# Kernel tuning notes

Measured on AMD Instinct MI355X. Metric: run time of the kernel, lower is better.

Reference implementation:

```python
import jax, jax.numpy as jnp
import numpy as np

N = 100_000   # nodes
E = 1_600_000 # edges
IN, H, OUT = 128, 128, 128
G = 64        # graphs in batch
EPS = 1e-5    # batchnorm eps


def setup_inputs() -> dict:
    key = jax.random.key(0)
    ks = jax.random.split(key, 16)
    x = jax.random.normal(ks[0], (N, IN), dtype=jnp.float32)
    edge_index = jax.random.randint(ks[1], (2, E), 0, N, dtype=jnp.int32)
    batch = jnp.sort(jax.random.randint(ks[2], (N,), 0, G, dtype=jnp.int32))
    def lin(k, fi, fo):
        return jax.random.normal(k, (fi, fo), dtype=jnp.float32) / np.sqrt(fi).astype(np.float32)
    inp = {
        'x': x, 'edge_index': edge_index, 'batch': batch,
        'W1': lin(ks[3], IN, H), 'b1': jnp.zeros((H,), jnp.float32),
        'g1': jnp.ones((H,), jnp.float32), 'beta1': jnp.zeros((H,), jnp.float32),
        'W2': lin(ks[4], H, H), 'b2': jnp.zeros((H,), jnp.float32),
        'g2': jnp.ones((H,), jnp.float32), 'beta2': jnp.zeros((H,), jnp.float32),
        'W3': lin(ks[5], H, H), 'b3': jnp.zeros((H,), jnp.float32),
        'g3': jnp.ones((H,), jnp.float32), 'beta3': jnp.zeros((H,), jnp.float32),
        'fc_w': lin(ks[6], H, OUT), 'fc_b': jnp.zeros((OUT,), jnp.float32),
    }
    return inp


def _gcn_prep(edge_index):
    # add self loops, compute symmetric normalization (shared across layers)
    loop = jnp.arange(N, dtype=edge_index.dtype)
    row = jnp.concatenate([edge_index[0], loop])  # source
    col = jnp.concatenate([edge_index[1], loop])  # target
    deg = jax.ops.segment_sum(jnp.ones_like(col, dtype=jnp.float32), col, num_segments=N)
    dinv = jnp.where(deg > 0, jax.lax.rsqrt(deg), 0.0)
    norm = dinv[row] * dinv[col]  # (E+N,)
    return row, col, norm


def _gcn_bn_relu(h, W, b, g, beta, row, col, norm):
    hw = h @ W                                           # (N, H)
    msg = norm[:, None] * hw[row]                        # gather + scale
    h = jax.ops.segment_sum(msg, col, num_segments=N) + b  # scatter-add
    # BatchNorm1d (training-mode batch statistics, biased var)
    mu = jnp.mean(h, axis=0)
    var = jnp.mean(jnp.square(h - mu), axis=0)
    h = g * (h - mu) * jax.lax.rsqrt(var + EPS) + beta
    return jax.nn.relu(h)


def reference(x, edge_index, batch, W1, b1, g1, beta1, W2, b2, g2, beta2,
              W3, b3, g3, beta3, fc_w, fc_b):
    row, col, norm = _gcn_prep(edge_index)
    h = _gcn_bn_relu(x, W1, b1, g1, beta1, row, col, norm)
    h = _gcn_bn_relu(h, W2, b2, g2, beta2, row, col, norm)
    h = _gcn_bn_relu(h, W3, b3, g3, beta3, row, col, norm)
    # global_mean_pool over batch assignment
    sums = jax.ops.segment_sum(h, batch, num_segments=G)
    cnt = jax.ops.segment_sum(jnp.ones((N,), jnp.float32), batch, num_segments=G)
    pooled = sums / jnp.maximum(cnt, 1.0)[:, None]       # (G, H)
    return pooled @ fc_w + fc_b                          # (G, OUT)
```

## Files before the change

kernel.cpp:

```cpp
#include <hip/hip_runtime.h>

#define NN 100000
#define EE 1600000
#define HH 128
#define GG 64
#define TOT (EE + NN)
#define PSPLIT 8
#define NB 782
#define BCAP 4096
#define FCHUNK 4096

typedef __attribute__((ext_vector_type(8))) short s16x8;
typedef __attribute__((ext_vector_type(4))) float f32x4;

__device__ __forceinline__ unsigned short f2bf(float f) {
    unsigned u = __float_as_uint(f);
    u = u + 0x7FFFu + ((u >> 16) & 1u);
    return (unsigned short)(u >> 16);
}


__global__ __launch_bounds__(256) void setup_kernel(const float* __restrict__ x,
                                                    const int* __restrict__ batch,
                                                    const float* __restrict__ W0,
                                                    const float* __restrict__ W1,
                                                    const float* __restrict__ W2,
                                                    unsigned* __restrict__ Xbf,
                                                    int* __restrict__ cursor,
                                                    int* __restrict__ gstart, int* __restrict__ gend,
                                                    float* __restrict__ poolsum,
                                                    unsigned short* __restrict__ Wt) {
    int i = blockIdx.x * 256 + threadIdx.x;
    if (i < NN * 64) {
        float2 v = ((const float2*)x)[i];
        Xbf[i] = (unsigned)f2bf(v.x) | ((unsigned)f2bf(v.y) << 16);
    }
    if (i < NB) cursor[i] = i * BCAP;
    if (i < GG * HH) poolsum[i] = 0.f;
    if (i < GG) {
        int lo = 0, hi = NN;
        while (lo < hi) { int m = (lo + hi) >> 1; if (batch[m] < i) lo = m + 1; else hi = m; }
        int s = lo;
        lo = 0; hi = NN;
        while (lo < hi) { int m = (lo + hi) >> 1; if (batch[m] < i + 1) lo = m + 1; else hi = m; }
        gstart[i] = s;
        gend[i] = lo;
    }
    if (i < 3 * HH * HH) {
        int l = i >> 14, r = i & 16383;
        const float* W = (l == 0) ? W0 : (l == 1) ? W1 : W2;
        int k = r >> 7, n = r & 127;
        int dst = ((((n >> 4) * 16 + (k >> 5) * 4 + ((k >> 3) & 3)) * 16) + (n & 15)) * 8 + (k & 7);
        Wt[l * HH * HH + dst] = f2bf(W[r]);
    }
}

__global__ __launch_bounds__(256) void bfill2_kernel(const int* __restrict__ ei, int* cursor,
                                                     unsigned* __restrict__ ebuf) {
    __shared__ int h[NB];
    __shared__ int lbase[NB];
    int tid = threadIdx.x;
    size_t e0 = (size_t)blockIdx.x * FCHUNK;
    for (int i = tid; i < NB; i += 256) h[i] = 0;
    __syncthreads();
    unsigned r[16], c[16];
#pragma unroll
    for (int k = 0; k < 16; ++k) {
        size_t e = e0 + (size_t)k * 256 + tid;
        unsigned rr = 0xFFFFFFFFu, cc = 0;
        if (e < EE) {
            rr = (unsigned)ei[e];
            cc = (unsigned)ei[EE + e];
            if (rr >= NN || cc >= NN) rr = 0xFFFFFFFFu;
        }
        r[k] = rr; c[k] = cc;
        if (rr != 0xFFFFFFFFu) atomicAdd(&h[cc >> 7], 1);
    }
    __syncthreads();
    for (int i = tid; i < NB; i += 256) {
        int cnt = h[i];
        lbase[i] = cnt ? atomicAdd(&cursor[i], cnt) : 0;
    }
    __syncthreads();
    for (int i = tid; i < NB; i += 256) h[i] = 0;
    __syncthreads();
#pragma unroll
    for (int k = 0; k < 16; ++k) {
        if (r[k] != 0xFFFFFFFFu) {
            unsigned cc = c[k];
            int b = cc >> 7;
            int slot = lbase[b] + atomicAdd(&h[b], 1);
            if (slot >= b * BCAP && slot < (b + 1) * BCAP)
                ebuf[slot] = (r[k] << 7) | (cc & 127u);
        }
    }
}

__global__ void bscan_kernel(const int* __restrict__ cursor, int* __restrict__ bucketSlotStart,
                             int* __restrict__ col_start) {
    __shared__ int ss[1024];
    int t = threadIdx.x;
    int ec = 0, nc = 0;
    if (t < NB) {
        ec = min(max(cursor[t] - t * BCAP, 0), BCAP);
        nc = min(128, NN - t * 128);
    }
    ss[t] = ec + nc;
    __syncthreads();
    for (int off = 1; off < 1024; off <<= 1) {
        int a = 0;
        if (t >= off) a = ss[t - off];
        __syncthreads();
        ss[t] += a;
        __syncthreads();
    }
    if (t < NB) bucketSlotStart[t] = ss[t] - (ec + nc);
    if (t == NB - 1) col_start[NN] = ss[t];
}

__global__ __launch_bounds__(256) void bproc_kernel(const unsigned* __restrict__ ebuf,
                                                    const int* __restrict__ cursor,
                                                    const int* __restrict__ bucketSlotStart,
                                                    int* __restrict__ col_start,
                                                    float* __restrict__ dinv,
                                                    int* __restrict__ srcv) {
    __shared__ unsigned s_e[BCAP];
    __shared__ int s_cnt[128], s_scan[128], s_cur[128];
    int b = blockIdx.x;
    int tid = threadIdx.x;
    int n0 = b * 128;
    int nb = min(128, NN - n0);
    int est = b * BCAP;
    int ecnt = min(max(cursor[b] - est, 0), BCAP);
    if (tid < 128) s_cnt[tid] = 0;
    __syncthreads();
    for (int i = tid; i < ecnt; i += 256) {
        unsigned v = ebuf[est + i];
        s_e[i] = v;
        atomicAdd(&s_cnt[v & 127u], 1);
    }
    __syncthreads();
    int myc = 0;
    if (tid < 128) {
        myc = (tid < nb) ? s_cnt[tid] + 1 : 0;
        s_scan[tid] = myc;
    }
    __syncthreads();
    for (int off = 1; off < 128; off <<= 1) {
        int a = 0;
        if (tid < 128 && tid >= off) a = s_scan[tid - off];
        __syncthreads();
        if (tid < 128) s_scan[tid] += a;
        __syncthreads();
    }
    if (tid < nb) {
        int slotbase = bucketSlotStart[b] + s_scan[tid] - myc;
        col_start[n0 + tid] = slotbase;
        dinv[n0 + tid] = rsqrtf((float)(s_cnt[tid] + 1));
        srcv[slotbase] = n0 + tid;
        s_cur[tid] = slotbase + 1;
    }
    __syncthreads();
    for (int i = tid; i < ecnt; i += 256) {
        unsigned v = s_e[i];
        int slot = atomicAdd(&s_cur[v & 127u], 1);
        srcv[slot] = (int)(v >> 7);
    }
}


__global__ __launch_bounds__(256) void agg_kernel(const uint4* __restrict__ Xbf4,
                                                  const int* __restrict__ col_start,
                                                  const int* __restrict__ srcv,
                                                  const float* __restrict__ dinv,
                                                  unsigned short* __restrict__ Abf,
                                                  float* __restrict__ gsum,
                                                  float* __restrict__ gsq) {
    if (blockIdx.x == 0 && threadIdx.x < HH) {
        gsum[threadIdx.x] = 0.f;
        gsq[threadIdx.x] = 0.f;
    }
    int wv = (int)((blockIdx.x * blockDim.x + threadIdx.x) >> 6);
    int lane = threadIdx.x & 63;
    int half = lane >> 5;
    int node = 2 * wv + half;
    if (2 * wv >= NN) return;
    bool valid = node < NN;
    int s0 = 0, s1 = 0;
    float dd = 0.f;
    if (valid) { s0 = col_start[node]; s1 = col_start[node + 1]; dd = dinv[node]; }
    int lane31 = lane & 31;
    int qh = (lane >> 4) & 1;
    int l16 = lane & 15;
    float acc[8];
#pragma unroll
    for (int j = 0; j < 8; ++j) acc[j] = 0.f;

    for (int base = s0; base < s1; base += 32) {
        int cnt = min(32, s1 - base);
        int msrc = 0;
        float mw = 0.f;
        if (lane31 < cnt) { msrc = srcv[base + lane31]; mw = dinv[msrc] * dd; }
        int rounds = (cnt + 1) >> 1;
        int rp = ((rounds + 5) / 6) * 6;
        for (int p = 0; p < rp; p += 6) {
            uint4 u[6];
            float w[6];
#pragma unroll
            for (int k = 0; k < 6; ++k) {
                int idx = (p + k) * 2 + qh;
                int sl = half * 32 + min(idx, 31);
                int src = __shfl(msrc, sl);
                float wk = __shfl(mw, sl);
                if (idx > 31) wk = 0.f;
                w[k] = wk;
                u[k] = Xbf4[(size_t)src * 16 + l16];
            }
#pragma unroll
            for (int k = 0; k < 6; ++k) {
                acc[0] += w[k] * __uint_as_float(u[k].x << 16);
                acc[1] += w[k] * __uint_as_float(u[k].x & 0xFFFF0000u);
                acc[2] += w[k] * __uint_as_float(u[k].y << 16);
                acc[3] += w[k] * __uint_as_float(u[k].y & 0xFFFF0000u);
                acc[4] += w[k] * __uint_as_float(u[k].z << 16);
                acc[5] += w[k] * __uint_as_float(u[k].z & 0xFFFF0000u);
                acc[6] += w[k] * __uint_as_float(u[k].w << 16);
                acc[7] += w[k] * __uint_as_float(u[k].w & 0xFFFF0000u);
            }
        }
    }
#pragma unroll
    for (int j = 0; j < 8; ++j) acc[j] += __shfl_xor(acc[j], 16);
    if ((lane & 16) == 0 && valid) {
        uint4 pk;
        pk.x = (unsigned)f2bf(acc[0]) | ((unsigned)f2bf(acc[1]) << 16);
        pk.y = (unsigned)f2bf(acc[2]) | ((unsigned)f2bf(acc[3]) << 16);
        pk.z = (unsigned)f2bf(acc[4]) | ((unsigned)f2bf(acc[5]) << 16);
        pk.w = (unsigned)f2bf(acc[6]) | ((unsigned)f2bf(acc[7]) << 16);
        ((uint4*)Abf)[(size_t)node * 16 + l16] = pk;
    }
}

__global__ __launch_bounds__(256) void gemm_stats_kernel(const unsigned short* __restrict__ Abf,
                                                         const unsigned short* __restrict__ Wf,
                                                         const float* __restrict__ bias,
                                                         float* __restrict__ gsum,
                                                         float* __restrict__ gsq) {
    __shared__ float ssum[HH], ssq[HH];
    int tid = threadIdx.x;
    if (tid < HH) { ssum[tid] = 0.f; ssq[tid] = 0.f; }
    __syncthreads();

    int lane = tid & 63;
    int wave = tid >> 6;
    int mcol = lane & 15;
    int quad = lane >> 4;
    int rowbase = blockIdx.x * 128 + wave * 32;
    int row0 = rowbase + mcol;
    int row1 = row0 + 16;

    f32x4 acc[2][8];
#pragma unroll
    for (int mt = 0; mt < 2; ++mt)
#pragma unroll
        for (int nt = 0; nt < 8; ++nt) acc[mt][nt] = (f32x4){0.f, 0.f, 0.f, 0.f};

    s16x8 zf = {0, 0, 0, 0, 0, 0, 0, 0};
#pragma unroll
    for (int ks = 0; ks < 4; ++ks) {
        int k0 = ks * 32 + quad * 8;
        s16x8 a0 = (row0 < NN) ? *(const s16x8*)(Abf + (size_t)row0 * HH + k0) : zf;
        s16x8 a1 = (row1 < NN) ? *(const s16x8*)(Abf + (size_t)row1 * HH + k0) : zf;
#pragma unroll
        for (int nt = 0; nt < 8; ++nt) {
            s16x8 b = *(const s16x8*)(Wf + (((nt * 16 + ks * 4 + quad) * 16 + mcol) << 3));
            acc[0][nt] = __builtin_amdgcn_mfma_f32_16x16x32_bf16(a0, b, acc[0][nt], 0, 0, 0);
            acc[1][nt] = __builtin_amdgcn_mfma_f32_16x16x32_bf16(a1, b, acc[1][nt], 0, 0, 0);
        }
    }

    float s[8], sq[8];
#pragma unroll
    for (int nt = 0; nt < 8; ++nt) { s[nt] = 0.f; sq[nt] = 0.f; }
#pragma unroll
    for (int mt = 0; mt < 2; ++mt) {
        int rbase = rowbase + mt * 16 + quad * 4;
#pragma unroll
        for (int nt = 0; nt < 8; ++nt) {
            float bv = bias[nt * 16 + mcol];
            f32x4 a = acc[mt][nt];
#pragma unroll
            for (int reg = 0; reg < 4; ++reg) {
                if (rbase + reg < NN) {
                    float h = a[reg] + bv;
                    s[nt] += h; sq[nt] += h * h;
                }
            }
        }
    }
#pragma unroll
    for (int nt = 0; nt < 8; ++nt) {
        float v = s[nt];  v += __shfl_xor(v, 16);  v += __shfl_xor(v, 32);
        float w = sq[nt]; w += __shfl_xor(w, 16);  w += __shfl_xor(w, 32);
        if (quad == 0) {
            atomicAdd(&ssum[nt * 16 + mcol], v);
            atomicAdd(&ssq[nt * 16 + mcol], w);
        }
    }
    __syncthreads();
    if (tid < HH) {
        atomicAdd(&gsum[tid], ssum[tid]);
        atomicAdd(&gsq[tid], ssq[tid]);
    }
}

__global__ __launch_bounds__(256) void gemm_apply_kernel(const unsigned short* __restrict__ Abf,
                                                         const unsigned short* __restrict__ Wf,
                                                         const float* __restrict__ bias,
                                                         const float* __restrict__ gsum,
                                                         const float* __restrict__ gsq,
                                                         const float* __restrict__ g,
                                                         const float* __restrict__ beta,
                                                         unsigned short* __restrict__ Xb16) {
    __shared__ float asc[HH], bsh[HH];
    int tid = threadIdx.x;
    if (tid < HH) {
        float mu = gsum[tid] * (1.f / (float)NN);
        float var = fmaxf(gsq[tid] * (1.f / (float)NN) - mu * mu, 0.f);
        float a = g[tid] * rsqrtf(var + 1e-5f);
        asc[tid] = a;
        bsh[tid] = a * (bias[tid] - mu) + beta[tid];
    }
    __syncthreads();

    int lane = tid & 63;
    int wave = tid >> 6;
    int mcol = lane & 15;
    int quad = lane >> 4;
    int rowbase = blockIdx.x * 128 + wave * 32;
    int row0 = rowbase + mcol;
    int row1 = row0 + 16;

    f32x4 acc[2][8];
#pragma unroll
    for (int mt = 0; mt < 2; ++mt)
#pragma unroll
        for (int nt = 0; nt < 8; ++nt) acc[mt][nt] = (f32x4){0.f, 0.f, 0.f, 0.f};

    s16x8 zf = {0, 0, 0, 0, 0, 0, 0, 0};
#pragma unroll
    for (int ks = 0; ks < 4; ++ks) {
        int k0 = ks * 32 + quad * 8;
        s16x8 a0 = (row0 < NN) ? *(const s16x8*)(Abf + (size_t)row0 * HH + k0) : zf;
        s16x8 a1 = (row1 < NN) ? *(const s16x8*)(Abf + (size_t)row1 * HH + k0) : zf;
#pragma unroll
        for (int nt = 0; nt < 8; ++nt) {
            s16x8 b = *(const s16x8*)(Wf + (((nt * 16 + ks * 4 + quad) * 16 + mcol) << 3));
            acc[0][nt] = __builtin_amdgcn_mfma_f32_16x16x32_bf16(a0, b, acc[0][nt], 0, 0, 0);
            acc[1][nt] = __builtin_amdgcn_mfma_f32_16x16x32_bf16(a1, b, acc[1][nt], 0, 0, 0);
        }
    }

#pragma unroll
    for (int mt = 0; mt < 2; ++mt) {
        int rbase = rowbase + mt * 16 + quad * 4;
#pragma unroll
        for (int nt = 0; nt < 8; ++nt) {
            int col = nt * 16 + mcol;
            float av = asc[col], bv = bsh[col];
            f32x4 a = acc[mt][nt];
#pragma unroll
            for (int reg = 0; reg < 4; ++reg) {
                int r = rbase + reg;
                if (r < NN) {
                    float o = fmaxf(av * a[reg] + bv, 0.f);
                    Xb16[(size_t)r * HH + col] = f2bf(o);
                }
            }
        }
    }
}


__global__ void pool_kernel(const unsigned* __restrict__ Xbf, const int* __restrict__ gstart,
                            const int* __restrict__ gend, float* __restrict__ poolsum) {
    int g = blockIdx.x;
    int sp = blockIdx.y;
    int t = threadIdx.x;
    int s = gstart[g], e = gend[g];
    if (e <= s) return;
    int len = e - s;
    int chunk = (len + PSPLIT - 1) / PSPLIT;
    int cs = s + sp * chunk;
    int ce = min(cs + chunk, e);
    if (cs >= ce) return;
    float2 acc = make_float2(0.f, 0.f);
    for (int i = cs; i < ce; ++i) {
        unsigned u = Xbf[(size_t)i * 64 + t];
        acc.x += __uint_as_float(u << 16);
        acc.y += __uint_as_float(u & 0xFFFF0000u);
    }
    atomicAdd(&poolsum[g * HH + 2 * t], acc.x);
    atomicAdd(&poolsum[g * HH + 2 * t + 1], acc.y);
}

__global__ void fc_kernel(const float* __restrict__ poolsum, const int* __restrict__ gstart,
                          const int* __restrict__ gend, const float* __restrict__ fc_w,
                          const float* __restrict__ fc_b, float* __restrict__ out) {
    int g = blockIdx.x;
    int o = threadIdx.x;
    int cnt = gend[g] - gstart[g];
    float inv = (cnt > 0) ? (1.f / (float)cnt) : 0.f;
    float acc = fc_b[o];
    for (int k = 0; k < HH; ++k) acc += (poolsum[g * HH + k] * inv) * fc_w[k * HH + o];
    out[g * HH + o] = acc;
}


extern "C" void kernel_launch(void* const* d_in, const int* in_sizes, int n_in,
                              void* d_out, int out_size, void* d_ws, size_t ws_size,
                              hipStream_t stream) {
    const float* x     = (const float*)d_in[0];
    const int*   ei    = (const int*)d_in[1];
    const int*   batch = (const int*)d_in[2];
    const float* Wl[3]    = {(const float*)d_in[3], (const float*)d_in[7], (const float*)d_in[11]};
    const float* bl[3]    = {(const float*)d_in[4], (const float*)d_in[8], (const float*)d_in[12]};
    const float* gl[3]    = {(const float*)d_in[5], (const float*)d_in[9], (const float*)d_in[13]};
    const float* betal[3] = {(const float*)d_in[6], (const float*)d_in[10], (const float*)d_in[14]};
    const float* fc_w = (const float*)d_in[15];
    const float* fc_b = (const float*)d_in[16];
    float* out = (float*)d_out;

    char* ws = (char*)d_ws;
    size_t off = 0;
    auto take = [&](size_t n) -> void* {
        void* p = ws + off;
        off = (off + n + 255) & ~(size_t)255;
        return p;
    };
    int*   bucketSlotStart = (int*)take((size_t)NB * 4);
    int*   cursor          = (int*)take((size_t)NB * 4);
    unsigned* ebuf         = (unsigned*)take((size_t)NB * BCAP * 4);
    int*   col_start       = (int*)take((size_t)(NN + 1) * 4);
    float* dinv            = (float*)take((size_t)NN * 4);
    int*   srcv            = (int*)take((size_t)TOT * 4);
    float* gsum            = (float*)take(HH * 4);
    float* gsq             = (float*)take(HH * 4);
    int*   gstart          = (int*)take(GG * 4);
    int*   gend            = (int*)take(GG * 4);
    float* poolsum         = (float*)take((size_t)GG * HH * 4);
    unsigned short* wt     = (unsigned short*)take((size_t)3 * HH * HH * 2);
    unsigned* Xbf          = (unsigned*)take((size_t)NN * 64 * 4);
    unsigned short* Abf    = (unsigned short*)take((size_t)NN * HH * 2);

    setup_kernel<<<(NN * 64 + 255) / 256, 256, 0, stream>>>(x, batch, Wl[0], Wl[1], Wl[2],
                                                            Xbf, cursor, gstart, gend, poolsum, wt);
    bfill2_kernel<<<(EE + FCHUNK - 1) / FCHUNK, 256, 0, stream>>>(ei, cursor, ebuf);
    bscan_kernel<<<1, 1024, 0, stream>>>(cursor, bucketSlotStart, col_start);
    bproc_kernel<<<NB, 256, 0, stream>>>(ebuf, cursor, bucketSlotStart, col_start, dinv, srcv);

    const int aggBlocks = (((NN + 1) / 2) * 64 + 255) / 256;
    for (int l = 0; l < 3; ++l) {
        const unsigned short* W = wt + (size_t)l * HH * HH;
        agg_kernel<<<aggBlocks, 256, 0, stream>>>((const uint4*)Xbf, col_start, srcv,
                                                  dinv, Abf, gsum, gsq);
        gemm_stats_kernel<<<(NN + 127) / 128, 256, 0, stream>>>(Abf, W, bl[l], gsum, gsq);
        gemm_apply_kernel<<<(NN + 127) / 128, 256, 0, stream>>>(Abf, W, bl[l], gsum, gsq,
                                                                gl[l], betal[l],
                                                                (unsigned short*)Xbf);
    }

    pool_kernel<<<dim3(GG, PSPLIT), 64, 0, stream>>>(Xbf, gstart, gend, poolsum);
    fc_kernel<<<GG, 128, 0, stream>>>(poolsum, gstart, gend, fc_w, fc_b, out);
}
```

Baseline: 550.3 us.

## Build CSR via global degree atomics and direct atomic scatter

Replaces the bucketed edge-buffer CSR construction with a global atomic degree count fused into setup, a block-level scan, a per-node prefix pass, and an atomic scatter of sources into CSR slots. It removes the intermediate ebuf round trip and its fixed-capacity buckets. In exchange it uses global atomics on 100K counters, which may contend, and edge order within rows becomes nondeterministic. The single-block scan now serially sums degrees per thread.

```diff
diff --git a/kernel.cpp b/kernel.cpp
--- a/kernel.cpp
+++ b/kernel.cpp
@@ -7,8 +7,6 @@
 #define TOT (EE + NN)
 #define PSPLIT 8
 #define NB 782
-#define BCAP 4096
-#define FCHUNK 4096
 
 typedef __attribute__((ext_vector_type(8))) short s16x8;
 typedef __attribute__((ext_vector_type(4))) float f32x4;
@@ -21,12 +19,13 @@
 
 
 __global__ __launch_bounds__(256) void setup_kernel(const float* __restrict__ x,
+                                                    const int* __restrict__ ei,
                                                     const int* __restrict__ batch,
                                                     const float* __restrict__ W0,
                                                     const float* __restrict__ W1,
                                                     const float* __restrict__ W2,
                                                     unsigned* __restrict__ Xbf,
-                                                    int* __restrict__ cursor,
+                                                    int* __restrict__ deg,
                                                     int* __restrict__ gstart, int* __restrict__ gend,
                                                     float* __restrict__ poolsum,
                                                     unsigned short* __restrict__ Wt) {
@@ -35,7 +34,10 @@
         float2 v = ((const float2*)x)[i];
         Xbf[i] = (unsigned)f2bf(v.x) | ((unsigned)f2bf(v.y) << 16);
     }
-    if (i < NB) cursor[i] = i * BCAP;
+    if (i < EE) {
+        unsigned r = (unsigned)ei[i], c = (unsigned)ei[EE + i];
+        if (r < NN && c < NN) atomicAdd(&deg[c], 1);
+    }
     if (i < GG * HH) poolsum[i] = 0.f;
     if (i < GG) {
         int lo = 0, hi = NN;
@@ -55,57 +57,17 @@
     }
 }
 
-__global__ __launch_bounds__(256) void bfill2_kernel(const int* __restrict__ ei, int* cursor,
-                                                     unsigned* __restrict__ ebuf) {
-    __shared__ int h[NB];
-    __shared__ int lbase[NB];
-    int tid = threadIdx.x;
-    size_t e0 = (size_t)blockIdx.x * FCHUNK;
-    for (int i = tid; i < NB; i += 256) h[i] = 0;
-    __syncthreads();
-    unsigned r[16], c[16];
-#pragma unroll
-    for (int k = 0; k < 16; ++k) {
-        size_t e = e0 + (size_t)k * 256 + tid;
-        unsigned rr = 0xFFFFFFFFu, cc = 0;
-        if (e < EE) {
-            rr = (unsigned)ei[e];
-            cc = (unsigned)ei[EE + e];
-            if (rr >= NN || cc >= NN) rr = 0xFFFFFFFFu;
-        }
-        r[k] = rr; c[k] = cc;
-        if (rr != 0xFFFFFFFFu) atomicAdd(&h[cc >> 7], 1);
-    }
-    __syncthreads();
-    for (int i = tid; i < NB; i += 256) {
-        int cnt = h[i];
-        lbase[i] = cnt ? atomicAdd(&cursor[i], cnt) : 0;
-    }
-    __syncthreads();
-    for (int i = tid; i < NB; i += 256) h[i] = 0;
-    __syncthreads();
-#pragma unroll
-    for (int k = 0; k < 16; ++k) {
-        if (r[k] != 0xFFFFFFFFu) {
-            unsigned cc = c[k];
-            int b = cc >> 7;
-            int slot = lbase[b] + atomicAdd(&h[b], 1);
-            if (slot >= b * BCAP && slot < (b + 1) * BCAP)
-                ebuf[slot] = (r[k] << 7) | (cc & 127u);
-        }
-    }
-}
-
-__global__ void bscan_kernel(const int* __restrict__ cursor, int* __restrict__ bucketSlotStart,
-                             int* __restrict__ col_start) {
+__global__ void bscan2_kernel(const int* __restrict__ deg, int* __restrict__ bucketSlotStart,
+                              int* __restrict__ col_start) {
     __shared__ int ss[1024];
     int t = threadIdx.x;
-    int ec = 0, nc = 0;
+    int sum = 0;
     if (t < NB) {
-        ec = min(max(cursor[t] - t * BCAP, 0), BCAP);
-        nc = min(128, NN - t * 128);
-    }
-    ss[t] = ec + nc;
+        int n0 = t * 128;
+        int nb = min(128, NN - n0);
+        for (int j = 0; j < nb; ++j) sum += deg[n0 + j] + 1;
+    }
+    ss[t] = sum;
     __syncthreads();
     for (int off = 1; off < 1024; off <<= 1) {
         int a = 0;
@@ -114,57 +76,49 @@
         ss[t] += a;
         __syncthreads();
     }
-    if (t < NB) bucketSlotStart[t] = ss[t] - (ec + nc);
+    if (t < NB) bucketSlotStart[t] = ss[t] - sum;
     if (t == NB - 1) col_start[NN] = ss[t];
 }
 
-__global__ __launch_bounds__(256) void bproc_kernel(const unsigned* __restrict__ ebuf,
-                                                    const int* __restrict__ cursor,
+__global__ __launch_bounds__(128) void bprep_kernel(const int* __restrict__ deg,
                                                     const int* __restrict__ bucketSlotStart,
                                                     int* __restrict__ col_start,
                                                     float* __restrict__ dinv,
-                                                    int* __restrict__ srcv) {
-    __shared__ unsigned s_e[BCAP];
-    __shared__ int s_cnt[128], s_scan[128], s_cur[128];
+                                                    int* __restrict__ srcv,
+                                                    int* __restrict__ cur) {
+    __shared__ int s_scan[128];
     int b = blockIdx.x;
     int tid = threadIdx.x;
-    int n0 = b * 128;
-    int nb = min(128, NN - n0);
-    int est = b * BCAP;
-    int ecnt = min(max(cursor[b] - est, 0), BCAP);
-    if (tid < 128) s_cnt[tid] = 0;
-    __syncthreads();
-    for (int i = tid; i < ecnt; i += 256) {
-        unsigned v = ebuf[est + i];
-        s_e[i] = v;
-        atomicAdd(&s_cnt[v & 127u], 1);
-    }
-    __syncthreads();
-    int myc = 0;
-    if (tid < 128) {
-        myc = (tid < nb) ? s_cnt[tid] + 1 : 0;
-        s_scan[tid] = myc;
-    }
+    int n = b * 128 + tid;
+    int myc = (n < NN) ? deg[n] + 1 : 0;
+    s_scan[tid] = myc;
     __syncthreads();
     for (int off = 1; off < 128; off <<= 1) {
         int a = 0;
-        if (tid < 128 && tid >= off) a = s_scan[tid - off];
+        if (tid >= off) a = s_scan[tid - off];
         __syncthreads();
-        if (tid < 128) s_scan[tid] += a;
+        s_scan[tid] += a;
         __syncthreads();
     }
-    if (tid < nb) {
+    if (n < NN) {
         int slotbase = bucketSlotStart[b] + s_scan[tid] - myc;
-        col_start[n0 + tid] = slotbase;
-        dinv[n0 + tid] = rsqrtf((float)(s_cnt[tid] + 1));
-        srcv[slotbase] = n0 + tid;
-        s_cur[tid] = slotbase + 1;
-    }
-    __syncthreads();
-    for (int i = tid; i < ecnt; i += 256) {
-        unsigned v = s_e[i];
-        int slot = atomicAdd(&s_cur[v & 127u], 1);
-        srcv[slot] = (int)(v >> 7);
+        col_start[n] = slotbase;
+        dinv[n] = rsqrtf((float)myc);
+        srcv[slotbase] = n;
+        cur[n] = slotbase + 1;
+    }
+}
+
+__global__ __launch_bounds__(256) void scatter_kernel(const int* __restrict__ ei,
+                                                      int* __restrict__ cur,
+                                                      int* __restrict__ srcv) {
+    int stride = gridDim.x * 256;
+    for (int e = blockIdx.x * 256 + threadIdx.x; e < EE; e += stride) {
+        unsigned r = (unsigned)ei[e], c = (unsigned)ei[EE + e];
+        if (r < NN && c < NN) {
+            int slot = atomicAdd(&cur[c], 1);
+            srcv[slot] = (int)r;
+        }
     }
 }
 
@@ -439,8 +393,8 @@
         return p;
     };
     int*   bucketSlotStart = (int*)take((size_t)NB * 4);
-    int*   cursor          = (int*)take((size_t)NB * 4);
-    unsigned* ebuf         = (unsigned*)take((size_t)NB * BCAP * 4);
+    int*   deg             = (int*)take((size_t)NN * 4);
+    int*   cur             = (int*)take((size_t)NN * 4);
     int*   col_start       = (int*)take((size_t)(NN + 1) * 4);
     float* dinv            = (float*)take((size_t)NN * 4);
     int*   srcv            = (int*)take((size_t)TOT * 4);
@@ -453,11 +407,12 @@
     unsigned* Xbf          = (unsigned*)take((size_t)NN * 64 * 4);
     unsigned short* Abf    = (unsigned short*)take((size_t)NN * HH * 2);
 
-    setup_kernel<<<(NN * 64 + 255) / 256, 256, 0, stream>>>(x, batch, Wl[0], Wl[1], Wl[2],
-                                                            Xbf, cursor, gstart, gend, poolsum, wt);
-    bfill2_kernel<<<(EE + FCHUNK - 1) / FCHUNK, 256, 0, stream>>>(ei, cursor, ebuf);
-    bscan_kernel<<<1, 1024, 0, stream>>>(cursor, bucketSlotStart, col_start);
-    bproc_kernel<<<NB, 256, 0, stream>>>(ebuf, cursor, bucketSlotStart, col_start, dinv, srcv);
+    hipMemsetAsync(deg, 0, (size_t)NN * 4, stream);
+    setup_kernel<<<(NN * 64 + 255) / 256, 256, 0, stream>>>(x, ei, batch, Wl[0], Wl[1], Wl[2],
+                                                            Xbf, deg, gstart, gend, poolsum, wt);
+    bscan2_kernel<<<1, 1024, 0, stream>>>(deg, bucketSlotStart, col_start);
+    bprep_kernel<<<NB, 128, 0, stream>>>(deg, bucketSlotStart, col_start, dinv, srcv, cur);
+    scatter_kernel<<<2048, 256, 0, stream>>>(ei, cur, srcv);
 
     const int aggBlocks = (((NN + 1) / 2) * 64 + 255) / 256;
     for (int l = 0; l < 3; ++l) {
```

After: 723.2 us. +31.4%, slower.

## Fuse neighbor aggregation with GEMM batch-stats and pooling with final FC

Applied to the files above, without the earlier changes.

Each aggregation block now gathers neighbor sums for its 128 nodes and then immediately runs the MFMA GEMM to accumulate batchnorm statistics, removing a separate kernel launch and letting the GEMM read freshly written rows. Per-layer stats buffers are zeroed once in setup. Mean pooling and the final linear layer are merged into one kernel without atomics. The aggregation grid shrinks sharply, so each block processes nodes sequentially, which may reduce latency hiding and increase load imbalance.

```diff
diff --git a/kernel.cpp b/kernel.cpp
--- a/kernel.cpp
+++ b/kernel.cpp
@@ -5,7 +5,6 @@
 #define HH 128
 #define GG 64
 #define TOT (EE + NN)
-#define PSPLIT 8
 #define NB 782
 #define BCAP 4096
 #define FCHUNK 4096
@@ -28,7 +27,7 @@
                                                     unsigned* __restrict__ Xbf,
                                                     int* __restrict__ cursor,
                                                     int* __restrict__ gstart, int* __restrict__ gend,
-                                                    float* __restrict__ poolsum,
+                                                    float* __restrict__ gsum, float* __restrict__ gsq,
                                                     unsigned short* __restrict__ Wt) {
     int i = blockIdx.x * 256 + threadIdx.x;
     if (i < NN * 64) {
@@ -36,7 +35,7 @@
         Xbf[i] = (unsigned)f2bf(v.x) | ((unsigned)f2bf(v.y) << 16);
     }
     if (i < NB) cursor[i] = i * BCAP;
-    if (i < GG * HH) poolsum[i] = 0.f;
+    if (i < 3 * HH) { gsum[i] = 0.f; gsq[i] = 0.f; }
     if (i < GG) {
         int lo = 0, hi = NN;
         while (lo < hi) { int m = (lo + hi) >> 1; if (batch[m] < i) lo = m + 1; else hi = m; }
@@ -169,101 +168,94 @@
 }
 
 
-__global__ __launch_bounds__(256) void agg_kernel(const uint4* __restrict__ Xbf4,
-                                                  const int* __restrict__ col_start,
-                                                  const int* __restrict__ srcv,
-                                                  const float* __restrict__ dinv,
-                                                  unsigned short* __restrict__ Abf,
-                                                  float* __restrict__ gsum,
-                                                  float* __restrict__ gsq) {
-    if (blockIdx.x == 0 && threadIdx.x < HH) {
-        gsum[threadIdx.x] = 0.f;
-        gsq[threadIdx.x] = 0.f;
-    }
-    int wv = (int)((blockIdx.x * blockDim.x + threadIdx.x) >> 6);
-    int lane = threadIdx.x & 63;
+__global__ __launch_bounds__(256) void aggstats_kernel(const uint4* __restrict__ Xbf4,
+                                                       const int* __restrict__ col_start,
+                                                       const int* __restrict__ srcv,
+                                                       const float* __restrict__ dinv,
+                                                       unsigned short* __restrict__ Abf,
+                                                       const unsigned short* __restrict__ Wf,
+                                                       const float* __restrict__ bias,
+                                                       float* __restrict__ gsum,
+                                                       float* __restrict__ gsq) {
+    __shared__ float ssum[HH], ssq[HH];
+    int tid = threadIdx.x;
+    if (tid < HH) { ssum[tid] = 0.f; ssq[tid] = 0.f; }
+
+    int lane = tid & 63;
+    int wave = tid >> 6;
     int half = lane >> 5;
-    int node = 2 * wv + half;
-    if (2 * wv >= NN) return;
-    bool valid = node < NN;
-    int s0 = 0, s1 = 0;
-    float dd = 0.f;
-    if (valid) { s0 = col_start[node]; s1 = col_start[node + 1]; dd = dinv[node]; }
     int lane31 = lane & 31;
     int qh = (lane >> 4) & 1;
     int l16 = lane & 15;
-    float acc[8];
-#pragma unroll
-    for (int j = 0; j < 8; ++j) acc[j] = 0.f;
-
-    for (int base = s0; base < s1; base += 32) {
-        int cnt = min(32, s1 - base);
-        int msrc = 0;
-        float mw = 0.f;
-        if (lane31 < cnt) { msrc = srcv[base + lane31]; mw = dinv[msrc] * dd; }
-        int rounds = (cnt + 1) >> 1;
-        int rp = ((rounds + 5) / 6) * 6;
-        for (int p = 0; p < rp; p += 6) {
-            uint4 u[6];
-            float w[6];
-#pragma unroll
-            for (int k = 0; k < 6; ++k) {
-                int idx = (p + k) * 2 + qh;
-                int sl = half * 32 + min(idx, 31);
-                int src = __shfl(msrc, sl);
-                float wk = __shfl(mw, sl);
-                if (idx > 31) wk = 0.f;
-                w[k] = wk;
-                u[k] = Xbf4[(size_t)src * 16 + l16];
+    int blkrow = blockIdx.x * 128;
+
+    for (int round = 0; round < 16; ++round) {
+        int node = blkrow + round * 8 + wave * 2 + half;
+        bool valid = node < NN;
+        int s0 = 0, s1 = 0;
+        float dd = 0.f;
+        if (valid) { s0 = col_start[node]; s1 = col_start[node + 1]; dd = dinv[node]; }
+        float acc[8];
+#pragma unroll
+        for (int j = 0; j < 8; ++j) acc[j] = 0.f;
+
+        for (int base = s0; base < s1; base += 32) {
+            int cnt = min(32, s1 - base);
+            int msrc = 0;
+            float mw = 0.f;
+            if (lane31 < cnt) { msrc = srcv[base + lane31]; mw = dinv[msrc] * dd; }
+            int rounds = (cnt + 1) >> 1;
+            int rp = ((rounds + 5) / 6) * 6;
+            for (int p = 0; p < rp; p += 6) {
+                uint4 u[6];
+                float w[6];
+#pragma unroll
+                for (int k = 0; k < 6; ++k) {
+                    int idx = (p + k) * 2 + qh;
+                    int sl = half * 32 + min(idx, 31);
+                    int src = __shfl(msrc, sl);
+                    float wk = __shfl(mw, sl);
+                    if (idx > 31) wk = 0.f;
+                    w[k] = wk;
+                    u[k] = Xbf4[(size_t)src * 16 + l16];
+                }
+#pragma unroll
+                for (int k = 0; k < 6; ++k) {
+                    acc[0] += w[k] * __uint_as_float(u[k].x << 16);
+                    acc[1] += w[k] * __uint_as_float(u[k].x & 0xFFFF0000u);
+                    acc[2] += w[k] * __uint_as_float(u[k].y << 16);
+                    acc[3] += w[k] * __uint_as_float(u[k].y & 0xFFFF0000u);
+                    acc[4] += w[k] * __uint_as_float(u[k].z << 16);
+                    acc[5] += w[k] * __uint_as_float(u[k].z & 0xFFFF0000u);
+                    acc[6] += w[k] * __uint_as_float(u[k].w << 16);
+                    acc[7] += w[k] * __uint_as_float(u[k].w & 0xFFFF0000u);
+                }
             }
-#pragma unroll
-            for (int k = 0; k < 6; ++k) {
-                acc[0] += w[k] * __uint_as_float(u[k].x << 16);
-                acc[1] += w[k] * __uint_as_float(u[k].x & 0xFFFF0000u);
-                acc[2] += w[k] * __uint_as_float(u[k].y << 16);
-                acc[3] += w[k] * __uint_as_float(u[k].y & 0xFFFF0000u);
-                acc[4] += w[k] * __uint_as_float(u[k].z << 16);
-                acc[5] += w[k] * __uint_as_float(u[k].z & 0xFFFF0000u);
-                acc[6] += w[k] * __uint_as_float(u[k].w << 16);
-                acc[7] += w[k] * __uint_as_float(u[k].w & 0xFFFF0000u);
-            }
-        }
-    }
-#pragma unroll
-    for (int j = 0; j < 8; ++j) acc[j] += __shfl_xor(acc[j], 16);
-    if ((lane & 16) == 0 && valid) {
-        uint4 pk;
-        pk.x = (unsigned)f2bf(acc[0]) | ((unsigned)f2bf(acc[1]) << 16);
-        pk.y = (unsigned)f2bf(acc[2]) | ((unsigned)f2bf(acc[3]) << 16);
-        pk.z = (unsigned)f2bf(acc[4]) | ((unsigned)f2bf(acc[5]) << 16);
-        pk.w = (unsigned)f2bf(acc[6]) | ((unsigned)f2bf(acc[7]) << 16);
-        ((uint4*)Abf)[(size_t)node * 16 + l16] = pk;
-    }
-}
-
-__global__ __launch_bounds__(256) void gemm_stats_kernel(const unsigned short* __restrict__ Abf,
-                                                         const unsigned short* __restrict__ Wf,
-                                                         const float* __restrict__ bias,
-                                                         float* __restrict__ gsum,
-                                                         float* __restrict__ gsq) {
-    __shared__ float ssum[HH], ssq[HH];
-    int tid = threadIdx.x;
-    if (tid < HH) { ssum[tid] = 0.f; ssq[tid] = 0.f; }
-    __syncthreads();
-
-    int lane = tid & 63;
-    int wave = tid >> 6;
+        }
+#pragma unroll
+        for (int j = 0; j < 8; ++j) acc[j] += __shfl_xor(acc[j], 16);
+        if ((lane & 16) == 0 && valid) {
+            uint4 pk;
+            pk.x = (unsigned)f2bf(acc[0]) | ((unsigned)f2bf(acc[1]) << 16);
+            pk.y = (unsigned)f2bf(acc[2]) | ((unsigned)f2bf(acc[3]) << 16);
+            pk.z = (unsigned)f2bf(acc[4]) | ((unsigned)f2bf(acc[5]) << 16);
+            pk.w = (unsigned)f2bf(acc[6]) | ((unsigned)f2bf(acc[7]) << 16);
+            ((uint4*)Abf)[(size_t)node * 16 + l16] = pk;
+        }
+    }
+    __syncthreads();
+
     int mcol = lane & 15;
     int quad = lane >> 4;
-    int rowbase = blockIdx.x * 128 + wave * 32;
+    int rowbase = blkrow + wave * 32;
     int row0 = rowbase + mcol;
     int row1 = row0 + 16;
 
-    f32x4 acc[2][8];
+    f32x4 acc2[2][8];
 #pragma unroll
     for (int mt = 0; mt < 2; ++mt)
 #pragma unroll
-        for (int nt = 0; nt < 8; ++nt) acc[mt][nt] = (f32x4){0.f, 0.f, 0.f, 0.f};
+        for (int nt = 0; nt < 8; ++nt) acc2[mt][nt] = (f32x4){0.f, 0.f, 0.f, 0.f};
 
     s16x8 zf = {0, 0, 0, 0, 0, 0, 0, 0};
 #pragma unroll
@@ -274,8 +266,8 @@
 #pragma unroll
         for (int nt = 0; nt < 8; ++nt) {
             s16x8 b = *(const s16x8*)(Wf + (((nt * 16 + ks * 4 + quad) * 16 + mcol) << 3));
-            acc[0][nt] = __builtin_amdgcn_mfma_f32_16x16x32_bf16(a0, b, acc[0][nt], 0, 0, 0);
-            acc[1][nt] = __builtin_amdgcn_mfma_f32_16x16x32_bf16(a1, b, acc[1][nt], 0, 0, 0);
+            acc2[0][nt] = __builtin_amdgcn_mfma_f32_16x16x32_bf16(a0, b, acc2[0][nt], 0, 0, 0);
+            acc2[1][nt] = __builtin_amdgcn_mfma_f32_16x16x32_bf16(a1, b, acc2[1][nt], 0, 0, 0);
         }
     }
 
@@ -288,7 +280,7 @@
 #pragma unroll
         for (int nt = 0; nt < 8; ++nt) {
             float bv = bias[nt * 16 + mcol];
-            f32x4 a = acc[mt][nt];
+            f32x4 a = acc2[mt][nt];
 #pragma unroll
             for (int reg = 0; reg < 4; ++reg) {
                 if (rbase + reg < NN) {
@@ -382,38 +374,42 @@
 }
 
 
-__global__ void pool_kernel(const unsigned* __restrict__ Xbf, const int* __restrict__ gstart,
-                            const int* __restrict__ gend, float* __restrict__ poolsum) {
+__global__ __launch_bounds__(256) void poolfc_kernel(const unsigned* __restrict__ Xbf,
+                                                     const int* __restrict__ gstart,
+                                                     const int* __restrict__ gend,
+                                                     const float* __restrict__ fc_w,
+                                                     const float* __restrict__ fc_b,
+                                                     float* __restrict__ out) {
+    __shared__ float sredx[256], sredy[256];
+    __shared__ float pooled[HH];
     int g = blockIdx.x;
-    int sp = blockIdx.y;
     int t = threadIdx.x;
     int s = gstart[g], e = gend[g];
-    if (e <= s) return;
-    int len = e - s;
-    int chunk = (len + PSPLIT - 1) / PSPLIT;
-    int cs = s + sp * chunk;
-    int ce = min(cs + chunk, e);
-    if (cs >= ce) return;
-    float2 acc = make_float2(0.f, 0.f);
-    for (int i = cs; i < ce; ++i) {
-        unsigned u = Xbf[(size_t)i * 64 + t];
-        acc.x += __uint_as_float(u << 16);
-        acc.y += __uint_as_float(u & 0xFFFF0000u);
-    }
-    atomicAdd(&poolsum[g * HH + 2 * t], acc.x);
-    atomicAdd(&poolsum[g * HH + 2 * t + 1], acc.y);
-}
-
-__global__ void fc_kernel(const float* __restrict__ poolsum, const int* __restrict__ gstart,
-                          const int* __restrict__ gend, const float* __restrict__ fc_w,
-                          const float* __restrict__ fc_b, float* __restrict__ out) {
-    int g = blockIdx.x;
-    int o = threadIdx.x;
-    int cnt = gend[g] - gstart[g];
-    float inv = (cnt > 0) ? (1.f / (float)cnt) : 0.f;
-    float acc = fc_b[o];
-    for (int k = 0; k < HH; ++k) acc += (poolsum[g * HH + k] * inv) * fc_w[k * HH + o];
-    out[g * HH + o] = acc;
+    int cp = t & 63;
+    int rs = t >> 6;
+    float ax = 0.f, ay = 0.f;
+    for (int i = s + rs; i < e; i += 4) {
+        unsigned u = Xbf[(size_t)i * 64 + cp];
+        ax += __uint_as_float(u << 16);
+        ay += __uint_as_float(u & 0xFFFF0000u);
+    }
+    sredx[t] = ax;
+    sredy[t] = ay;
+    __syncthreads();
+    if (t < 64) {
+        float px = 0.f, py = 0.f;
+#pragma unroll
+        for (int r = 0; r < 4; ++r) { px += sredx[r * 64 + t]; py += sredy[r * 64 + t]; }
+        float inv = (e > s) ? (1.f / (float)(e - s)) : 0.f;
+        pooled[2 * t] = px * inv;
+        pooled[2 * t + 1] = py * inv;
+    }
+    __syncthreads();
+    if (t < HH) {
+        float acc = fc_b[t];
+        for (int k = 0; k < HH; ++k) acc += pooled[k] * fc_w[k * HH + t];
+        out[g * HH + t] = acc;
+    }
 }
 
 
@@ -444,32 +440,31 @@
     int*   col_start       = (int*)take((size_t)(NN + 1) * 4);
     float* dinv            = (float*)take((size_t)NN * 4);
     int*   srcv            = (int*)take((size_t)TOT * 4);
-    float* gsum            = (float*)take(HH * 4);
-    float* gsq             = (float*)take(HH * 4);
+    float* gsum            = (float*)take((size_t)3 * HH * 4);
+    float* gsq             = (float*)take((size_t)3 * HH * 4);
     int*   gstart          = (int*)take(GG * 4);
     int*   gend            = (int*)take(GG * 4);
-    float* poolsum         = (float*)take((size_t)GG * HH * 4);
     unsigned short* wt     = (unsigned short*)take((size_t)3 * HH * HH * 2);
     unsigned* Xbf          = (unsigned*)take((size_t)NN * 64 * 4);
     unsigned short* Abf    = (unsigned short*)take((size_t)NN * HH * 2);
 
     setup_kernel<<<(NN * 64 + 255) / 256, 256, 0, stream>>>(x, batch, Wl[0], Wl[1], Wl[2],
-                                                            Xbf, cursor, gstart, gend, poolsum, wt);
+                                                            Xbf, cursor, gstart, gend,
+                                                            gsum, gsq, wt);
     bfill2_kernel<<<(EE + FCHUNK - 1) / FCHUNK, 256, 0, stream>>>(ei, cursor, ebuf);
     bscan_kernel<<<1, 1024, 0, stream>>>(cursor, bucketSlotStart, col_start);
     bproc_kernel<<<NB, 256, 0, stream>>>(ebuf, cursor, bucketSlotStart, col_start, dinv, srcv);
 
-    const int aggBlocks = (((NN + 1) / 2) * 64 + 255) / 256;
     for (int l = 0; l < 3; ++l) {
         const unsigned short* W = wt + (size_t)l * HH * HH;
-        agg_kernel<<<aggBlocks, 256, 0, stream>>>((const uint4*)Xbf, col_start, srcv,
-                                                  dinv, Abf, gsum, gsq);
-        gemm_stats_kernel<<<(NN + 127) / 128, 256, 0, stream>>>(Abf, W, bl[l], gsum, gsq);
-        gemm_apply_kernel<<<(NN + 127) / 128, 256, 0, stream>>>(Abf, W, bl[l], gsum, gsq,
+        float* gs = gsum + l * HH;
+        float* gq = gsq + l * HH;
+        aggstats_kernel<<<NB, 256, 0, stream>>>((const uint4*)Xbf, col_start, srcv, dinv,
+                                                Abf, W, bl[l], gs, gq);
+        gemm_apply_kernel<<<(NN + 127) / 128, 256, 0, stream>>>(Abf, W, bl[l], gs, gq,
                                                                 gl[l], betal[l],
                                                                 (unsigned short*)Xbf);
     }
 
-    pool_kernel<<<dim3(GG, PSPLIT), 64, 0, stream>>>(Xbf, gstart, gend, poolsum);
-    fc_kernel<<<GG, 128, 0, stream>>>(poolsum, gstart, gend, fc_w, fc_b, out);
-}
+    poolfc_kernel<<<GG, 256, 0, stream>>>(Xbf, gstart, gend, fc_w, fc_b, out);
+}
```

Result: slower. 644.3 us (+17.1%).
